# Kernel optimization log

Hardware: AMD Instinct MI355X
Metric: run time of the kernel (lower is better)

## Reference

```python
import jax, jax.numpy as jnp
import numpy as np

B, H, S, D = 4, 16, 2048, 128

def setup_inputs() -> dict:
    key = jax.random.key(0)
    k1, k2, k3, k4 = jax.random.split(key, 4)
    query = jax.random.normal(k1, (B, H, S, D), dtype=jnp.float32)
    key_t = jax.random.normal(k2, (B, H, S, D), dtype=jnp.float32)
    value = jax.random.normal(k3, (B, H, S, D), dtype=jnp.float32)
    mask = jax.random.randint(k4, (B, 1, S, S), 0, 2, dtype=jnp.int32)
    return {"query": query, "key": key_t, "value": value, "mask": mask}

def reference(query, key, value, mask):
    d_k = query.shape[-1]
    scale = d_k ** 0.5
    # [B,H,S,S] attention logits
    attn_logits = jnp.einsum('bhqd,bhkd->bhqk', query, key)
    neg_inf = jnp.finfo(attn_logits.dtype).min
    attn_logits = jnp.where(mask == 0, neg_inf, attn_logits)
    attn_weights = jax.nn.softmax(attn_logits / scale, axis=-1)
    # dropout is identity in eval/inference mode
    attn_output = jnp.einsum('bhqk,bhkd->bhqd', attn_weights, value)
    return attn_output, attn_weights
```

## Files before the change

kernel.cpp:

```cpp
#include <hip/hip_runtime.h>
#include <hip/hip_bf16.h>

namespace {

constexpr int Hn = 16;
constexpr int Sn = 2048;
constexpr int Dn = 128;
constexpr int BM = 64;
constexpr int BN = 64;
constexpr int THREADS = 256;
constexpr int NT = Sn / BN;
constexpr long long OUT0 = 4LL * 16 * 2048 * 128;

constexpr int QSTR = 136;
constexpr int VSTR = 68;

typedef short s16x4 __attribute__((ext_vector_type(4)));
typedef float f32x4 __attribute__((ext_vector_type(4)));

__device__ __forceinline__ unsigned short f2bu(float x) {
    return __bfloat16_as_ushort(__float2bfloat16(x));
}
__device__ __forceinline__ unsigned pk2(float lo, float hi) {
    return (unsigned)f2bu(lo) | ((unsigned)f2bu(hi) << 16);
}

__device__ __forceinline__ void k_issue(const float* __restrict__ g, int sc, int sr,
                                        float4* v) {
#pragma unroll
    for (int it = 0; it < 4; ++it) {
        const float4* gp = reinterpret_cast<const float4*>(
            g + (size_t)(sr + 16 * it) * Dn + sc * 8);
        v[2 * it]     = gp[0];
        v[2 * it + 1] = gp[1];
    }
}
__device__ __forceinline__ void k_write(unsigned short* lds, int sc, int sr,
                                        const float4* v) {
#pragma unroll
    for (int it = 0; it < 4; ++it) {
        const int r = sr + 16 * it;
        uint4 u;
        u.x = pk2(v[2 * it].x,     v[2 * it].y);
        u.y = pk2(v[2 * it].z,     v[2 * it].w);
        u.z = pk2(v[2 * it + 1].x, v[2 * it + 1].y);
        u.w = pk2(v[2 * it + 1].z, v[2 * it + 1].w);
        *reinterpret_cast<uint4*>(reinterpret_cast<char*>(lds) + r * (QSTR * 2) + sc * 16) = u;
    }
}

__device__ __forceinline__ void v_issue(const float* __restrict__ g, int tc, int kp,
                                        float4* v) {
#pragma unroll
    for (int it = 0; it < 4; ++it) {
        const int kr = 2 * (kp + 8 * it);
        v[2 * it]     = *reinterpret_cast<const float4*>(g + (size_t)kr * Dn + 4 * tc);
        v[2 * it + 1] = *reinterpret_cast<const float4*>(g + (size_t)(kr + 1) * Dn + 4 * tc);
    }
}
__device__ __forceinline__ void v_write(unsigned short* vt, int tc, int kp,
                                        const float4* v) {
#pragma unroll
    for (int it = 0; it < 4; ++it) {
        const int kr = 2 * (kp + 8 * it);
        const float a4[4] = {v[2 * it].x, v[2 * it].y, v[2 * it].z, v[2 * it].w};
        const float b4[4] = {v[2 * it + 1].x, v[2 * it + 1].y, v[2 * it + 1].z, v[2 * it + 1].w};
#pragma unroll
        for (int j = 0; j < 4; ++j) {
            const int d = 4 * tc + j;
            *reinterpret_cast<unsigned*>(reinterpret_cast<char*>(vt) + d * (VSTR * 2) + kr * 2)
                = pk2(a4[j], b4[j]);
        }
    }
}

struct SAcc { f32x4 t[4]; };

__global__ __launch_bounds__(THREADS)
void attn_fused(const float* __restrict__ Q, const float* __restrict__ K,
                const float* __restrict__ V, const int* __restrict__ M,
                float* __restrict__ out) {
    __shared__ __align__(16) unsigned short smem[8704 * 2 + BM * VSTR];
    unsigned short* bufA = smem;
    unsigned short* bufB = smem + 8704;
    unsigned short* wlds = smem + 17408;

    const int tid  = threadIdx.x;
    const int lane = tid & 63;
    const int wv   = tid >> 6;
    const int lr   = lane & 15;
    const int lg   = lane >> 4;

    const int bh    = blockIdx.y;
    const int b     = bh >> 4;
    const int qbase = blockIdx.x * BM;

    const float* Qg = Q + ((size_t)bh * Sn + qbase) * Dn;
    const float* Kg = K + (size_t)bh * Sn * Dn;
    const float* Vg = V + (size_t)bh * Sn * Dn;
    const int*   Mg = M + ((size_t)b * Sn + qbase) * Sn;
    float*       Og = out + ((size_t)bh * Sn + qbase) * Dn;
    float*       Wg = out + OUT0 + ((size_t)bh * Sn + qbase) * Sn;

    const float scl2 = 1.4426950408889634f / 11.313708498984761f;
    const int qrow = 16 * wv + 4 * lg;

    const int sc = tid & 15, sr = tid >> 4;
    const int tc = tid & 31, kp = tid >> 5;

    const int* mrow[4];
#pragma unroll
    for (int r = 0; r < 4; ++r) mrow[r] = Mg + (size_t)(qrow + r) * Sn + lr;

    {
        float4 qv[8], kv[8];
        k_issue(Qg, sc, sr, qv);
        k_issue(Kg, sc, sr, kv);
        k_write(bufB, sc, sr, qv);
        k_write(bufA, sc, sr, kv);
    }
    __syncthreads();
    s16x4 qf[8];
#pragma unroll
    for (int dsv = 0; dsv < 8; ++dsv)
        qf[dsv] = *reinterpret_cast<const s16x4*>(
            reinterpret_cast<const char*>(bufB) + (16 * wv + lr) * (QSTR * 2) + dsv * 32 + lg * 8);
    __syncthreads();

    const f32x4 zero = {0.f, 0.f, 0.f, 0.f};

    auto qk_tile = [&](const unsigned short* kb) -> SAcc {
        SAcc s;
#pragma unroll
        for (int t = 0; t < 4; ++t) s.t[t] = zero;
#pragma unroll
        for (int dsv = 0; dsv < 8; ++dsv) {
            const int koff = dsv * 32 + lg * 8;
#pragma unroll
            for (int t = 0; t < 4; ++t) {
                const s16x4 bb = *reinterpret_cast<const s16x4*>(
                    reinterpret_cast<const char*>(kb) + (16 * t + lr) * (QSTR * 2) + koff);
                s.t[t] = __builtin_amdgcn_mfma_f32_16x16x16bf16_1k(qf[dsv], bb, s.t[t], 0, 0, 0);
            }
        }
        return s;
    };

    float rs[4] = {0.f, 0.f, 0.f, 0.f};
    for (int t = 0; t < NT; ++t) {
        unsigned short* cur = (t & 1) ? bufB : bufA;
        unsigned short* nxt = (t & 1) ? bufA : bufB;
        float4 kv[8];
        const bool pre = (t + 1 < NT);
        if (pre) k_issue(Kg + (size_t)(t + 1) * BN * Dn, sc, sr, kv);

        int mv[16];
        const int kc = t * BN;
#pragma unroll
        for (int tt = 0; tt < 4; ++tt)
#pragma unroll
            for (int r = 0; r < 4; ++r) mv[4 * tt + r] = mrow[r][kc + 16 * tt];

        SAcc s = qk_tile(cur);
#pragma unroll
        for (int tt = 0; tt < 4; ++tt)
#pragma unroll
            for (int r = 0; r < 4; ++r)
                rs[r] += mv[4 * tt + r] ? __builtin_amdgcn_exp2f(s.t[tt][r] * scl2) : 0.f;

        if (pre) k_write(nxt, sc, sr, kv);
        __syncthreads();
    }

    float inv[4];
#pragma unroll
    for (int r = 0; r < 4; ++r) {
        float v = rs[r];
        v += __shfl_xor(v, 1);
        v += __shfl_xor(v, 2);
        v += __shfl_xor(v, 4);
        v += __shfl_xor(v, 8);
        inv[r] = 1.0f / v;
    }

    {
        float4 kv0[8], vv0[8];
        k_issue(Kg, sc, sr, kv0);
        v_issue(Vg, tc, kp, vv0);
        k_write(bufA, sc, sr, kv0);
        v_write(bufB, tc, kp, vv0);
    }
    __syncthreads();

    f32x4 oacc[8];
#pragma unroll
    for (int f = 0; f < 8; ++f) oacc[f] = zero;

    for (int t = 0; t < NT; ++t) {
        float4 kv[8], vv[8];
        const bool pre = (t + 1 < NT);
        if (pre) {
            k_issue(Kg + (size_t)(t + 1) * BN * Dn, sc, sr, kv);
            v_issue(Vg + (size_t)(t + 1) * BN * Dn, tc, kp, vv);
        }

        int mv[16];
        const int kc = t * BN;
#pragma unroll
        for (int tt = 0; tt < 4; ++tt)
#pragma unroll
            for (int r = 0; r < 4; ++r) mv[4 * tt + r] = mrow[r][kc + 16 * tt];

        SAcc s = qk_tile(bufA);

#pragma unroll
        for (int tt = 0; tt < 4; ++tt) {
#pragma unroll
            for (int r = 0; r < 4; ++r) {
                const float e = mv[4 * tt + r] ? __builtin_amdgcn_exp2f(s.t[tt][r] * scl2) : 0.f;
                const float w = e * inv[r];
                Wg[(size_t)(qrow + r) * Sn + kc + 16 * tt + lr] = w;
                reinterpret_cast<unsigned short*>(
                    reinterpret_cast<char*>(wlds) + (qrow + r) * (VSTR * 2))[16 * tt + lr] = f2bu(w);
            }
        }

#pragma unroll
        for (int kk = 0; kk < 4; ++kk) {
            const int koff = kk * 32 + lg * 8;
            const s16x4 aw = *reinterpret_cast<const s16x4*>(
                reinterpret_cast<const char*>(wlds) + (16 * wv + lr) * (VSTR * 2) + koff);
#pragma unroll
            for (int f = 0; f < 8; ++f) {
                const s16x4 bv = *reinterpret_cast<const s16x4*>(
                    reinterpret_cast<const char*>(bufB) + (16 * f + lr) * (VSTR * 2) + koff);
                oacc[f] = __builtin_amdgcn_mfma_f32_16x16x16bf16_1k(aw, bv, oacc[f], 0, 0, 0);
            }
        }
        __syncthreads();
        if (pre) {
            k_write(bufA, sc, sr, kv);
            v_write(bufB, tc, kp, vv);
        }
        __syncthreads();
    }

#pragma unroll
    for (int f = 0; f < 8; ++f) {
#pragma unroll
        for (int r = 0; r < 4; ++r) {
            Og[(size_t)(qrow + r) * Dn + 16 * f + lr] = oacc[f][r];
        }
    }
}

}

extern "C" void kernel_launch(void* const* d_in, const int* in_sizes, int n_in,
                              void* d_out, int out_size, void* d_ws, size_t ws_size,
                              hipStream_t stream) {
    (void)in_sizes; (void)n_in; (void)d_ws; (void)ws_size; (void)out_size;
    const float* Q = (const float*)d_in[0];
    const float* K = (const float*)d_in[1];
    const float* V = (const float*)d_in[2];
    const int*   M = (const int*)d_in[3];
    float* out = (float*)d_out;
    dim3 grid(Sn / BM, 4 * Hn);
    attn_fused<<<grid, THREADS, 0, stream>>>(Q, K, V, M, out);
}
```

Before: 1.006 ms.

## Shrink KV tile, bitpack mask in registers, double-buffer V, coalesce weight stores

Halves the key tile to 32 columns and adds double buffers for both K and V so one barrier per tile is enough. The mask is read once in the first pass and kept as bits in registers, so the second pass no longer reloads it from global memory. Attention weights are staged through LDS and written to global as coalesced float4 rows rather than scattered scalar stores. Block indices are remapped so blocks sharing a batch-head run close together, and launch bounds request three blocks per CU. The weights written to global now go through a bf16 round-trip, which costs some precision, and the smaller tiles add loop and barrier overhead.

New measurement: 1.510 ms. 1.5x slower.

```diff
diff --git a/kernel.cpp b/kernel.cpp
--- a/kernel.cpp
+++ b/kernel.cpp
@@ -3,17 +3,19 @@
 
 namespace {
 
-constexpr int Hn = 16;
 constexpr int Sn = 2048;
 constexpr int Dn = 128;
 constexpr int BM = 64;
-constexpr int BN = 64;
+constexpr int BN = 32;
 constexpr int THREADS = 256;
 constexpr int NT = Sn / BN;
-constexpr long long OUT0 = 4LL * 16 * 2048 * 128;
-
-constexpr int QSTR = 136;
-constexpr int VSTR = 68;
+constexpr long long OUT0 = 4LL * 16 * Sn * Dn;
+
+constexpr int KSTR = 136;
+constexpr int VSTR = 34;
+constexpr int KT = BN * KSTR;
+constexpr int VT = Dn * VSTR;
+constexpr int WT = BM * VSTR;
 
 typedef short s16x4 __attribute__((ext_vector_type(4)));
 typedef float f32x4 __attribute__((ext_vector_type(4)));
@@ -24,45 +26,48 @@
 __device__ __forceinline__ unsigned pk2(float lo, float hi) {
     return (unsigned)f2bu(lo) | ((unsigned)f2bu(hi) << 16);
 }
-
-__device__ __forceinline__ void k_issue(const float* __restrict__ g, int sc, int sr,
-                                        float4* v) {
-#pragma unroll
-    for (int it = 0; it < 4; ++it) {
+__device__ __forceinline__ float b2f(unsigned short u) {
+    union { unsigned u; float f; } v; v.u = (unsigned)u << 16; return v.f;
+}
+
+__device__ __forceinline__ void k_issue32(const float* __restrict__ g, int sc, int sr,
+                                          float4* v) {
+#pragma unroll
+    for (int it = 0; it < 2; ++it) {
         const float4* gp = reinterpret_cast<const float4*>(
             g + (size_t)(sr + 16 * it) * Dn + sc * 8);
         v[2 * it]     = gp[0];
         v[2 * it + 1] = gp[1];
     }
 }
-__device__ __forceinline__ void k_write(unsigned short* lds, int sc, int sr,
-                                        const float4* v) {
-#pragma unroll
-    for (int it = 0; it < 4; ++it) {
+__device__ __forceinline__ void k_write32(unsigned short* lds, int sc, int sr,
+                                          const float4* v) {
+#pragma unroll
+    for (int it = 0; it < 2; ++it) {
         const int r = sr + 16 * it;
         uint4 u;
         u.x = pk2(v[2 * it].x,     v[2 * it].y);
         u.y = pk2(v[2 * it].z,     v[2 * it].w);
         u.z = pk2(v[2 * it + 1].x, v[2 * it + 1].y);
         u.w = pk2(v[2 * it + 1].z, v[2 * it + 1].w);
-        *reinterpret_cast<uint4*>(reinterpret_cast<char*>(lds) + r * (QSTR * 2) + sc * 16) = u;
-    }
-}
-
-__device__ __forceinline__ void v_issue(const float* __restrict__ g, int tc, int kp,
-                                        float4* v) {
-#pragma unroll
-    for (int it = 0; it < 4; ++it) {
-        const int kr = 2 * (kp + 8 * it);
+        *reinterpret_cast<uint4*>(reinterpret_cast<char*>(lds) + r * (KSTR * 2) + sc * 16) = u;
+    }
+}
+
+__device__ __forceinline__ void v_issue32(const float* __restrict__ g, int tc, int kp,
+                                          float4* v) {
+#pragma unroll
+    for (int it = 0; it < 2; ++it) {
+        const int kr = 2 * kp + 16 * it;
         v[2 * it]     = *reinterpret_cast<const float4*>(g + (size_t)kr * Dn + 4 * tc);
         v[2 * it + 1] = *reinterpret_cast<const float4*>(g + (size_t)(kr + 1) * Dn + 4 * tc);
     }
 }
-__device__ __forceinline__ void v_write(unsigned short* vt, int tc, int kp,
-                                        const float4* v) {
-#pragma unroll
-    for (int it = 0; it < 4; ++it) {
-        const int kr = 2 * (kp + 8 * it);
+__device__ __forceinline__ void v_write32(unsigned short* vt, int tc, int kp,
+                                          const float4* v) {
+#pragma unroll
+    for (int it = 0; it < 2; ++it) {
+        const int kr = 2 * kp + 16 * it;
         const float a4[4] = {v[2 * it].x, v[2 * it].y, v[2 * it].z, v[2 * it].w};
         const float b4[4] = {v[2 * it + 1].x, v[2 * it + 1].y, v[2 * it + 1].z, v[2 * it + 1].w};
 #pragma unroll
@@ -74,16 +79,16 @@
     }
 }
 
-struct SAcc { f32x4 t[4]; };
-
-__global__ __launch_bounds__(THREADS)
+__global__ __launch_bounds__(THREADS, 3)
 void attn_fused(const float* __restrict__ Q, const float* __restrict__ K,
                 const float* __restrict__ V, const int* __restrict__ M,
                 float* __restrict__ out) {
-    __shared__ __align__(16) unsigned short smem[8704 * 2 + BM * VSTR];
-    unsigned short* bufA = smem;
-    unsigned short* bufB = smem + 8704;
-    unsigned short* wlds = smem + 17408;
+    __shared__ __align__(16) unsigned short smem[2 * KT + 2 * VT + WT];
+    unsigned short* kb0 = smem;
+    unsigned short* kb1 = smem + KT;
+    unsigned short* vb0 = smem + 2 * KT;
+    unsigned short* vb1 = smem + 2 * KT + VT;
+    unsigned short* wl  = smem + 2 * KT + 2 * VT;
 
     const int tid  = threadIdx.x;
     const int lane = tid & 63;
@@ -91,9 +96,13 @@
     const int lr   = lane & 15;
     const int lg   = lane >> 4;
 
-    const int bh    = blockIdx.y;
-    const int b     = bh >> 4;
-    const int qbase = blockIdx.x * BM;
+    const int wg = blockIdx.x;
+    const int x  = wg & 7;
+    const int j  = wg >> 3;
+    const int bh = 8 * x + (j & 7);
+    const int qt = j >> 3;
+    const int b  = bh >> 4;
+    const int qbase = qt * BM;
 
     const float* Qg = Q + ((size_t)bh * Sn + qbase) * Dn;
     const float* Kg = K + (size_t)bh * Sn * Dn;
@@ -113,63 +122,79 @@
     for (int r = 0; r < 4; ++r) mrow[r] = Mg + (size_t)(qrow + r) * Sn + lr;
 
     {
-        float4 qv[8], kv[8];
-        k_issue(Qg, sc, sr, qv);
-        k_issue(Kg, sc, sr, kv);
-        k_write(bufB, sc, sr, qv);
-        k_write(bufA, sc, sr, kv);
+        float4 q0[4], q1[4], kv[4];
+        k_issue32(Qg, sc, sr, q0);
+        k_issue32(Qg + 32 * Dn, sc, sr, q1);
+        k_issue32(Kg, sc, sr, kv);
+        k_write32(vb0, sc, sr, q0);
+        k_write32(vb1, sc, sr, q1);
+        k_write32(kb0, sc, sr, kv);
     }
     __syncthreads();
+
     s16x4 qf[8];
-#pragma unroll
-    for (int dsv = 0; dsv < 8; ++dsv)
-        qf[dsv] = *reinterpret_cast<const s16x4*>(
-            reinterpret_cast<const char*>(bufB) + (16 * wv + lr) * (QSTR * 2) + dsv * 32 + lg * 8);
+    {
+        const unsigned short* qsrc = (wv >= 2) ? vb1 : vb0;
+        const int qr = 16 * (wv & 1) + lr;
+#pragma unroll
+        for (int dsv = 0; dsv < 8; ++dsv)
+            qf[dsv] = *reinterpret_cast<const s16x4*>(
+                reinterpret_cast<const char*>(qsrc) + qr * (KSTR * 2) + dsv * 32 + lg * 8);
+    }
     __syncthreads();
 
     const f32x4 zero = {0.f, 0.f, 0.f, 0.f};
 
-    auto qk_tile = [&](const unsigned short* kb) -> SAcc {
-        SAcc s;
-#pragma unroll
-        for (int t = 0; t < 4; ++t) s.t[t] = zero;
-#pragma unroll
-        for (int dsv = 0; dsv < 8; ++dsv) {
-            const int koff = dsv * 32 + lg * 8;
-#pragma unroll
-            for (int t = 0; t < 4; ++t) {
-                const s16x4 bb = *reinterpret_cast<const s16x4*>(
-                    reinterpret_cast<const char*>(kb) + (16 * t + lr) * (QSTR * 2) + koff);
-                s.t[t] = __builtin_amdgcn_mfma_f32_16x16x16bf16_1k(qf[dsv], bb, s.t[t], 0, 0, 0);
+    float rs[4] = {0.f, 0.f, 0.f, 0.f};
+    unsigned mb[4][4];
+#pragma unroll
+    for (int r = 0; r < 4; ++r)
+#pragma unroll
+        for (int w = 0; w < 4; ++w) mb[r][w] = 0u;
+
+    {
+        unsigned short* kcur = kb0;
+        unsigned short* knxt = kb1;
+#pragma unroll
+        for (int w = 0; w < 4; ++w) {
+            for (int ti = 0; ti < 16; ++ti) {
+                const int to = 16 * w + ti;
+                const bool pre = (to < NT - 1);
+                float4 kv[4];
+                if (pre) k_issue32(Kg + (size_t)(to + 1) * BN * Dn, sc, sr, kv);
+
+                unsigned mvv[2][4];
+#pragma unroll
+                for (int t = 0; t < 2; ++t)
+#pragma unroll
+                    for (int r = 0; r < 4; ++r) {
+                        const unsigned m = (mrow[r][32 * to + 16 * t] != 0) ? 1u : 0u;
+                        mvv[t][r] = m;
+                        mb[r][w] |= m << (2 * ti + t);
+                    }
+
+                f32x4 s[2] = {zero, zero};
+#pragma unroll
+                for (int dsv = 0; dsv < 8; ++dsv) {
+                    const int koff = dsv * 32 + lg * 8;
+#pragma unroll
+                    for (int t = 0; t < 2; ++t) {
+                        const s16x4 bb = *reinterpret_cast<const s16x4*>(
+                            reinterpret_cast<const char*>(kcur) + (16 * t + lr) * (KSTR * 2) + koff);
+                        s[t] = __builtin_amdgcn_mfma_f32_16x16x16bf16_1k(qf[dsv], bb, s[t], 0, 0, 0);
+                    }
+                }
+#pragma unroll
+                for (int t = 0; t < 2; ++t)
+#pragma unroll
+                    for (int r = 0; r < 4; ++r)
+                        rs[r] += mvv[t][r] ? __builtin_amdgcn_exp2f(s[t][r] * scl2) : 0.f;
+
+                if (pre) k_write32(knxt, sc, sr, kv);
+                __syncthreads();
+                unsigned short* tmp = kcur; kcur = knxt; knxt = tmp;
             }
         }
-        return s;
-    };
-
-    float rs[4] = {0.f, 0.f, 0.f, 0.f};
-    for (int t = 0; t < NT; ++t) {
-        unsigned short* cur = (t & 1) ? bufB : bufA;
-        unsigned short* nxt = (t & 1) ? bufA : bufB;
-        float4 kv[8];
-        const bool pre = (t + 1 < NT);
-        if (pre) k_issue(Kg + (size_t)(t + 1) * BN * Dn, sc, sr, kv);
-
-        int mv[16];
-        const int kc = t * BN;
-#pragma unroll
-        for (int tt = 0; tt < 4; ++tt)
-#pragma unroll
-            for (int r = 0; r < 4; ++r) mv[4 * tt + r] = mrow[r][kc + 16 * tt];
-
-        SAcc s = qk_tile(cur);
-#pragma unroll
-        for (int tt = 0; tt < 4; ++tt)
-#pragma unroll
-            for (int r = 0; r < 4; ++r)
-                rs[r] += mv[4 * tt + r] ? __builtin_amdgcn_exp2f(s.t[tt][r] * scl2) : 0.f;
-
-        if (pre) k_write(nxt, sc, sr, kv);
-        __syncthreads();
     }
 
     float inv[4];
@@ -184,11 +209,11 @@
     }
 
     {
-        float4 kv0[8], vv0[8];
-        k_issue(Kg, sc, sr, kv0);
-        v_issue(Vg, tc, kp, vv0);
-        k_write(bufA, sc, sr, kv0);
-        v_write(bufB, tc, kp, vv0);
+        float4 kv[4], vv[4];
+        k_issue32(Kg, sc, sr, kv);
+        v_issue32(Vg, tc, kp, vv);
+        k_write32(kb0, sc, sr, kv);
+        v_write32(vb0, tc, kp, vv);
     }
     __syncthreads();
 
@@ -196,62 +221,88 @@
 #pragma unroll
     for (int f = 0; f < 8; ++f) oacc[f] = zero;
 
-    for (int t = 0; t < NT; ++t) {
-        float4 kv[8], vv[8];
-        const bool pre = (t + 1 < NT);
-        if (pre) {
-            k_issue(Kg + (size_t)(t + 1) * BN * Dn, sc, sr, kv);
-            v_issue(Vg + (size_t)(t + 1) * BN * Dn, tc, kp, vv);
-        }
-
-        int mv[16];
-        const int kc = t * BN;
-#pragma unroll
-        for (int tt = 0; tt < 4; ++tt)
-#pragma unroll
-            for (int r = 0; r < 4; ++r) mv[4 * tt + r] = mrow[r][kc + 16 * tt];
-
-        SAcc s = qk_tile(bufA);
-
-#pragma unroll
-        for (int tt = 0; tt < 4; ++tt) {
-#pragma unroll
-            for (int r = 0; r < 4; ++r) {
-                const float e = mv[4 * tt + r] ? __builtin_amdgcn_exp2f(s.t[tt][r] * scl2) : 0.f;
-                const float w = e * inv[r];
-                Wg[(size_t)(qrow + r) * Sn + kc + 16 * tt + lr] = w;
-                reinterpret_cast<unsigned short*>(
-                    reinterpret_cast<char*>(wlds) + (qrow + r) * (VSTR * 2))[16 * tt + lr] = f2bu(w);
+    {
+        unsigned short* kcur = kb0;
+        unsigned short* knxt = kb1;
+        unsigned short* vcur = vb0;
+        unsigned short* vnxt = vb1;
+        const int rowl = lane >> 2;
+        const int colg = lane & 3;
+#pragma unroll
+        for (int w = 0; w < 4; ++w) {
+            for (int ti = 0; ti < 16; ++ti) {
+                const int to = 16 * w + ti;
+                const int kc = 32 * to;
+                const bool pre = (to < NT - 1);
+                float4 kv[4], vv[4];
+                if (pre) {
+                    k_issue32(Kg + (size_t)(to + 1) * BN * Dn, sc, sr, kv);
+                    v_issue32(Vg + (size_t)(to + 1) * BN * Dn, tc, kp, vv);
+                }
+
+                f32x4 s[2] = {zero, zero};
+#pragma unroll
+                for (int dsv = 0; dsv < 8; ++dsv) {
+                    const int koff = dsv * 32 + lg * 8;
+#pragma unroll
+                    for (int t = 0; t < 2; ++t) {
+                        const s16x4 bb = *reinterpret_cast<const s16x4*>(
+                            reinterpret_cast<const char*>(kcur) + (16 * t + lr) * (KSTR * 2) + koff);
+                        s[t] = __builtin_amdgcn_mfma_f32_16x16x16bf16_1k(qf[dsv], bb, s[t], 0, 0, 0);
+                    }
+                }
+
+#pragma unroll
+                for (int t = 0; t < 2; ++t)
+#pragma unroll
+                    for (int r = 0; r < 4; ++r) {
+                        const unsigned mv = (mb[r][w] >> (2 * ti + t)) & 1u;
+                        const float e = mv ? __builtin_amdgcn_exp2f(s[t][r] * scl2) : 0.f;
+                        reinterpret_cast<unsigned short*>(
+                            reinterpret_cast<char*>(wl) + (qrow + r) * (VSTR * 2))[16 * t + lr]
+                            = f2bu(e * inv[r]);
+                    }
+
+#pragma unroll
+                for (int kk = 0; kk < 2; ++kk) {
+                    const int koff = kk * 32 + lg * 8;
+                    const s16x4 aw = *reinterpret_cast<const s16x4*>(
+                        reinterpret_cast<const char*>(wl) + (16 * wv + lr) * (VSTR * 2) + koff);
+#pragma unroll
+                    for (int f = 0; f < 8; ++f) {
+                        const s16x4 bv = *reinterpret_cast<const s16x4*>(
+                            reinterpret_cast<const char*>(vcur) + (16 * f + lr) * (VSTR * 2) + koff);
+                        oacc[f] = __builtin_amdgcn_mfma_f32_16x16x16bf16_1k(aw, bv, oacc[f], 0, 0, 0);
+                    }
+                }
+
+#pragma unroll
+                for (int i = 0; i < 2; ++i) {
+                    const ushort4 u = *reinterpret_cast<const ushort4*>(
+                        reinterpret_cast<const char*>(wl)
+                        + (16 * wv + rowl) * (VSTR * 2) + colg * 8 + 32 * i);
+                    float4 o;
+                    o.x = b2f(u.x); o.y = b2f(u.y); o.z = b2f(u.z); o.w = b2f(u.w);
+                    *reinterpret_cast<float4*>(
+                        Wg + (size_t)(16 * wv + rowl) * Sn + kc + colg * 4 + 16 * i) = o;
+                }
+
+                if (pre) {
+                    k_write32(knxt, sc, sr, kv);
+                    v_write32(vnxt, tc, kp, vv);
+                }
+                __syncthreads();
+                unsigned short* tmp = kcur; kcur = knxt; knxt = tmp;
+                tmp = vcur; vcur = vnxt; vnxt = tmp;
             }
         }
-
-#pragma unroll
-        for (int kk = 0; kk < 4; ++kk) {
-            const int koff = kk * 32 + lg * 8;
-            const s16x4 aw = *reinterpret_cast<const s16x4*>(
-                reinterpret_cast<const char*>(wlds) + (16 * wv + lr) * (VSTR * 2) + koff);
-#pragma unroll
-            for (int f = 0; f < 8; ++f) {
-                const s16x4 bv = *reinterpret_cast<const s16x4*>(
-                    reinterpret_cast<const char*>(bufB) + (16 * f + lr) * (VSTR * 2) + koff);
-                oacc[f] = __builtin_amdgcn_mfma_f32_16x16x16bf16_1k(aw, bv, oacc[f], 0, 0, 0);
-            }
-        }
-        __syncthreads();
-        if (pre) {
-            k_write(bufA, sc, sr, kv);
-            v_write(bufB, tc, kp, vv);
-        }
-        __syncthreads();
-    }
-
-#pragma unroll
-    for (int f = 0; f < 8; ++f) {
-#pragma unroll
-        for (int r = 0; r < 4; ++r) {
+    }
+
+#pragma unroll
+    for (int f = 0; f < 8; ++f)
+#pragma unroll
+        for (int r = 0; r < 4; ++r)
             Og[(size_t)(qrow + r) * Dn + 16 * f + lr] = oacc[f][r];
-        }
-    }
 }
 
 }
@@ -265,6 +316,5 @@
     const float* V = (const float*)d_in[2];
     const int*   M = (const int*)d_in[3];
     float* out = (float*)d_out;
-    dim3 grid(Sn / BM, 4 * Hn);
-    attn_fused<<<grid, THREADS, 0, stream>>>(Q, K, V, M, out);
-}
+    attn_fused<<<dim3(2048), dim3(THREADS), 0, stream>>>(Q, K, V, M, out);
+}
```

## Double query tile to 128 rows with 512 threads, fold scale into Q

Applied to the files above, without the earlier changes.

Each block now handles 128 query rows with 8 waves, so every K and V tile loaded into LDS serves twice as many rows and global K/V traffic per output halves. The softmax scale is pre-multiplied into Q during the bf16 conversion, and normalisation uses exp2(s - log2(sum)) instead of a multiply by the reciprocal. The LDS layout changes to one K buffer plus a transposed V buffer with a new stride, and launch bounds request 4 blocks per CU. Risks are higher register pressure and LDS use per block, fewer blocks in the grid, and slightly different bf16 rounding of the scaled Q.

Result: slower. 1.404 ms (+39.6%).

```diff
diff --git a/kernel.cpp b/kernel.cpp
--- a/kernel.cpp
+++ b/kernel.cpp
@@ -3,17 +3,19 @@
 
 namespace {
 
-constexpr int Hn = 16;
 constexpr int Sn = 2048;
 constexpr int Dn = 128;
-constexpr int BM = 64;
+constexpr int BM = 128;
 constexpr int BN = 64;
-constexpr int THREADS = 256;
+constexpr int THREADS = 512;
 constexpr int NT = Sn / BN;
-constexpr long long OUT0 = 4LL * 16 * 2048 * 128;
-
-constexpr int QSTR = 136;
-constexpr int VSTR = 68;
+constexpr long long OUT0 = 4LL * 16 * Sn * Dn;
+
+constexpr int KSTR = 136;
+constexpr int VSTR = 70;
+constexpr int KT = BN * KSTR;
+constexpr int VT = Dn * VSTR;
+constexpr int WT = BM * VSTR;
 
 typedef short s16x4 __attribute__((ext_vector_type(4)));
 typedef float f32x4 __attribute__((ext_vector_type(4)));
@@ -25,44 +27,57 @@
     return (unsigned)f2bu(lo) | ((unsigned)f2bu(hi) << 16);
 }
 
-__device__ __forceinline__ void k_issue(const float* __restrict__ g, int sc, int sr,
-                                        float4* v) {
-#pragma unroll
-    for (int it = 0; it < 4; ++it) {
+__device__ __forceinline__ void k_issue64(const float* __restrict__ g, int sc, int sr,
+                                          float4* v) {
+#pragma unroll
+    for (int it = 0; it < 2; ++it) {
         const float4* gp = reinterpret_cast<const float4*>(
-            g + (size_t)(sr + 16 * it) * Dn + sc * 8);
+            g + (size_t)(sr + 32 * it) * Dn + sc * 8);
         v[2 * it]     = gp[0];
         v[2 * it + 1] = gp[1];
     }
 }
-__device__ __forceinline__ void k_write(unsigned short* lds, int sc, int sr,
-                                        const float4* v) {
-#pragma unroll
-    for (int it = 0; it < 4; ++it) {
-        const int r = sr + 16 * it;
+__device__ __forceinline__ void k_write64(unsigned short* lds, int sc, int sr,
+                                          const float4* v) {
+#pragma unroll
+    for (int it = 0; it < 2; ++it) {
+        const int r = sr + 32 * it;
         uint4 u;
         u.x = pk2(v[2 * it].x,     v[2 * it].y);
         u.y = pk2(v[2 * it].z,     v[2 * it].w);
         u.z = pk2(v[2 * it + 1].x, v[2 * it + 1].y);
         u.w = pk2(v[2 * it + 1].z, v[2 * it + 1].w);
-        *reinterpret_cast<uint4*>(reinterpret_cast<char*>(lds) + r * (QSTR * 2) + sc * 16) = u;
-    }
-}
-
-__device__ __forceinline__ void v_issue(const float* __restrict__ g, int tc, int kp,
-                                        float4* v) {
-#pragma unroll
-    for (int it = 0; it < 4; ++it) {
-        const int kr = 2 * (kp + 8 * it);
+        *reinterpret_cast<uint4*>(reinterpret_cast<char*>(lds) + r * (KSTR * 2) + sc * 16) = u;
+    }
+}
+__device__ __forceinline__ void q_write64(unsigned short* lds, int sc, int sr,
+                                          const float4* v, float qs) {
+#pragma unroll
+    for (int it = 0; it < 2; ++it) {
+        const int r = sr + 32 * it;
+        uint4 u;
+        u.x = pk2(v[2 * it].x * qs,     v[2 * it].y * qs);
+        u.y = pk2(v[2 * it].z * qs,     v[2 * it].w * qs);
+        u.z = pk2(v[2 * it + 1].x * qs, v[2 * it + 1].y * qs);
+        u.w = pk2(v[2 * it + 1].z * qs, v[2 * it + 1].w * qs);
+        *reinterpret_cast<uint4*>(reinterpret_cast<char*>(lds) + r * (KSTR * 2) + sc * 16) = u;
+    }
+}
+
+__device__ __forceinline__ void v_issue64(const float* __restrict__ g, int tc, int kp,
+                                          float4* v) {
+#pragma unroll
+    for (int it = 0; it < 2; ++it) {
+        const int kr = 2 * kp + 32 * it;
         v[2 * it]     = *reinterpret_cast<const float4*>(g + (size_t)kr * Dn + 4 * tc);
         v[2 * it + 1] = *reinterpret_cast<const float4*>(g + (size_t)(kr + 1) * Dn + 4 * tc);
     }
 }
-__device__ __forceinline__ void v_write(unsigned short* vt, int tc, int kp,
-                                        const float4* v) {
-#pragma unroll
-    for (int it = 0; it < 4; ++it) {
-        const int kr = 2 * (kp + 8 * it);
+__device__ __forceinline__ void v_write64(unsigned short* vt, int tc, int kp,
+                                          const float4* v) {
+#pragma unroll
+    for (int it = 0; it < 2; ++it) {
+        const int kr = 2 * kp + 32 * it;
         const float a4[4] = {v[2 * it].x, v[2 * it].y, v[2 * it].z, v[2 * it].w};
         const float b4[4] = {v[2 * it + 1].x, v[2 * it + 1].y, v[2 * it + 1].z, v[2 * it + 1].w};
 #pragma unroll
@@ -74,16 +89,16 @@
     }
 }
 
-struct SAcc { f32x4 t[4]; };
-
-__global__ __launch_bounds__(THREADS)
+#define MFMA16(A, B, C) __builtin_amdgcn_mfma_f32_16x16x16bf16_1k((A), (B), (C), 0, 0, 0)
+
+__global__ __launch_bounds__(THREADS, 4)
 void attn_fused(const float* __restrict__ Q, const float* __restrict__ K,
                 const float* __restrict__ V, const int* __restrict__ M,
                 float* __restrict__ out) {
-    __shared__ __align__(16) unsigned short smem[8704 * 2 + BM * VSTR];
-    unsigned short* bufA = smem;
-    unsigned short* bufB = smem + 8704;
-    unsigned short* wlds = smem + 17408;
+    __shared__ __align__(16) unsigned short smem[KT + VT + WT];
+    unsigned short* kbuf = smem;
+    unsigned short* vt   = smem + KT;
+    unsigned short* wl   = smem + KT + VT;
 
     const int tid  = threadIdx.x;
     const int lane = tid & 63;
@@ -102,7 +117,7 @@
     float*       Og = out + ((size_t)bh * Sn + qbase) * Dn;
     float*       Wg = out + OUT0 + ((size_t)bh * Sn + qbase) * Sn;
 
-    const float scl2 = 1.4426950408889634f / 11.313708498984761f;
+    const float QS = 1.4426950408889634f / 11.313708498984761f;
     const int qrow = 16 * wv + 4 * lg;
 
     const int sc = tid & 15, sr = tid >> 4;
@@ -112,67 +127,72 @@
 #pragma unroll
     for (int r = 0; r < 4; ++r) mrow[r] = Mg + (size_t)(qrow + r) * Sn + lr;
 
-    {
-        float4 qv[8], kv[8];
-        k_issue(Qg, sc, sr, qv);
-        k_issue(Kg, sc, sr, kv);
-        k_write(bufB, sc, sr, qv);
-        k_write(bufA, sc, sr, kv);
-    }
-    __syncthreads();
+    const f32x4 zero = {0.f, 0.f, 0.f, 0.f};
+
+    float4 kv0[4];
+    {
+        float4 qlo[4], qhi[4];
+        k_issue64(Qg, sc, sr, qlo);
+        k_issue64(Qg + 64 * Dn, sc, sr, qhi);
+        k_issue64(Kg, sc, sr, kv0);
+        q_write64(kbuf, sc, sr, qlo, QS);
+        q_write64(vt,   sc, sr, qhi, QS);
+    }
+    __syncthreads();
+
     s16x4 qf[8];
-#pragma unroll
-    for (int dsv = 0; dsv < 8; ++dsv)
-        qf[dsv] = *reinterpret_cast<const s16x4*>(
-            reinterpret_cast<const char*>(bufB) + (16 * wv + lr) * (QSTR * 2) + dsv * 32 + lg * 8);
-    __syncthreads();
-
-    const f32x4 zero = {0.f, 0.f, 0.f, 0.f};
-
-    auto qk_tile = [&](const unsigned short* kb) -> SAcc {
-        SAcc s;
-#pragma unroll
-        for (int t = 0; t < 4; ++t) s.t[t] = zero;
-#pragma unroll
-        for (int dsv = 0; dsv < 8; ++dsv) {
-            const int koff = dsv * 32 + lg * 8;
-#pragma unroll
-            for (int t = 0; t < 4; ++t) {
-                const s16x4 bb = *reinterpret_cast<const s16x4*>(
-                    reinterpret_cast<const char*>(kb) + (16 * t + lr) * (QSTR * 2) + koff);
-                s.t[t] = __builtin_amdgcn_mfma_f32_16x16x16bf16_1k(qf[dsv], bb, s.t[t], 0, 0, 0);
-            }
-        }
-        return s;
-    };
+    {
+        const unsigned short* qsrc = (wv >= 4) ? vt : kbuf;
+        const int qr = 16 * (wv & 3) + lr;
+#pragma unroll
+        for (int dsv = 0; dsv < 8; ++dsv)
+            qf[dsv] = *reinterpret_cast<const s16x4*>(
+                reinterpret_cast<const char*>(qsrc) + qr * (KSTR * 2) + dsv * 32 + lg * 8);
+    }
+    __syncthreads();
+    k_write64(kbuf, sc, sr, kv0);
+    __syncthreads();
 
     float rs[4] = {0.f, 0.f, 0.f, 0.f};
-    for (int t = 0; t < NT; ++t) {
-        unsigned short* cur = (t & 1) ? bufB : bufA;
-        unsigned short* nxt = (t & 1) ? bufA : bufB;
-        float4 kv[8];
-        const bool pre = (t + 1 < NT);
-        if (pre) k_issue(Kg + (size_t)(t + 1) * BN * Dn, sc, sr, kv);
-
-        int mv[16];
-        const int kc = t * BN;
-#pragma unroll
-        for (int tt = 0; tt < 4; ++tt)
-#pragma unroll
-            for (int r = 0; r < 4; ++r) mv[4 * tt + r] = mrow[r][kc + 16 * tt];
-
-        SAcc s = qk_tile(cur);
-#pragma unroll
-        for (int tt = 0; tt < 4; ++tt)
-#pragma unroll
-            for (int r = 0; r < 4; ++r)
-                rs[r] += mv[4 * tt + r] ? __builtin_amdgcn_exp2f(s.t[tt][r] * scl2) : 0.f;
-
-        if (pre) k_write(nxt, sc, sr, kv);
-        __syncthreads();
-    }
-
-    float inv[4];
+    {
+        unsigned short* kcur = kbuf;
+        unsigned short* knxt = vt;
+        for (int t = 0; t < NT; ++t) {
+            const bool pre = (t + 1 < NT);
+            float4 kv[4];
+            if (pre) k_issue64(Kg + (size_t)(t + 1) * BN * Dn, sc, sr, kv);
+
+            int mv[16];
+            const int kc = t * BN;
+#pragma unroll
+            for (int tt = 0; tt < 4; ++tt)
+#pragma unroll
+                for (int r = 0; r < 4; ++r) mv[4 * tt + r] = mrow[r][kc + 16 * tt];
+
+            f32x4 s[4] = {zero, zero, zero, zero};
+#pragma unroll
+            for (int dsv = 0; dsv < 8; ++dsv) {
+                const int koff = dsv * 32 + lg * 8;
+#pragma unroll
+                for (int tt = 0; tt < 4; ++tt) {
+                    const s16x4 bb = *reinterpret_cast<const s16x4*>(
+                        reinterpret_cast<const char*>(kcur) + (16 * tt + lr) * (KSTR * 2) + koff);
+                    s[tt] = MFMA16(qf[dsv], bb, s[tt]);
+                }
+            }
+#pragma unroll
+            for (int tt = 0; tt < 4; ++tt)
+#pragma unroll
+                for (int r = 0; r < 4; ++r)
+                    rs[r] += mv[4 * tt + r] ? __builtin_amdgcn_exp2f(s[tt][r]) : 0.f;
+
+            if (pre) k_write64(knxt, sc, sr, kv);
+            __syncthreads();
+            unsigned short* tmp = kcur; kcur = knxt; knxt = tmp;
+        }
+    }
+
+    float li[4];
 #pragma unroll
     for (int r = 0; r < 4; ++r) {
         float v = rs[r];
@@ -180,15 +200,15 @@
         v += __shfl_xor(v, 2);
         v += __shfl_xor(v, 4);
         v += __shfl_xor(v, 8);
-        inv[r] = 1.0f / v;
-    }
-
-    {
-        float4 kv0[8], vv0[8];
-        k_issue(Kg, sc, sr, kv0);
-        v_issue(Vg, tc, kp, vv0);
-        k_write(bufA, sc, sr, kv0);
-        v_write(bufB, tc, kp, vv0);
+        li[r] = -__log2f(v);
+    }
+
+    {
+        float4 kv[4], vv[4];
+        k_issue64(Kg, sc, sr, kv);
+        v_issue64(Vg, tc, kp, vv);
+        k_write64(kbuf, sc, sr, kv);
+        v_write64(vt, tc, kp, vv);
     }
     __syncthreads();
 
@@ -197,31 +217,41 @@
     for (int f = 0; f < 8; ++f) oacc[f] = zero;
 
     for (int t = 0; t < NT; ++t) {
-        float4 kv[8], vv[8];
+        const int kc = t * BN;
         const bool pre = (t + 1 < NT);
+        float4 kv[4], vv[4];
         if (pre) {
-            k_issue(Kg + (size_t)(t + 1) * BN * Dn, sc, sr, kv);
-            v_issue(Vg + (size_t)(t + 1) * BN * Dn, tc, kp, vv);
+            k_issue64(Kg + (size_t)(t + 1) * BN * Dn, sc, sr, kv);
+            v_issue64(Vg + (size_t)(t + 1) * BN * Dn, tc, kp, vv);
         }
 
         int mv[16];
-        const int kc = t * BN;
 #pragma unroll
         for (int tt = 0; tt < 4; ++tt)
 #pragma unroll
             for (int r = 0; r < 4; ++r) mv[4 * tt + r] = mrow[r][kc + 16 * tt];
 
-        SAcc s = qk_tile(bufA);
+        f32x4 s[4] = {zero, zero, zero, zero};
+#pragma unroll
+        for (int dsv = 0; dsv < 8; ++dsv) {
+            const int koff = dsv * 32 + lg * 8;
+#pragma unroll
+            for (int tt = 0; tt < 4; ++tt) {
+                const s16x4 bb = *reinterpret_cast<const s16x4*>(
+                    reinterpret_cast<const char*>(kbuf) + (16 * tt + lr) * (KSTR * 2) + koff);
+                s[tt] = MFMA16(qf[dsv], bb, s[tt]);
+            }
+        }
 
 #pragma unroll
         for (int tt = 0; tt < 4; ++tt) {
 #pragma unroll
             for (int r = 0; r < 4; ++r) {
-                const float e = mv[4 * tt + r] ? __builtin_amdgcn_exp2f(s.t[tt][r] * scl2) : 0.f;
-                const float w = e * inv[r];
-                Wg[(size_t)(qrow + r) * Sn + kc + 16 * tt + lr] = w;
+                const float e = mv[4 * tt + r]
+                    ? __builtin_amdgcn_exp2f(s[tt][r] + li[r]) : 0.f;
+                Wg[(size_t)(qrow + r) * Sn + kc + 16 * tt + lr] = e;
                 reinterpret_cast<unsigned short*>(
-                    reinterpret_cast<char*>(wlds) + (qrow + r) * (VSTR * 2))[16 * tt + lr] = f2bu(w);
+                    reinterpret_cast<char*>(wl) + (qrow + r) * (VSTR * 2))[16 * tt + lr] = f2bu(e);
             }
         }
 
@@ -229,29 +259,28 @@
         for (int kk = 0; kk < 4; ++kk) {
             const int koff = kk * 32 + lg * 8;
             const s16x4 aw = *reinterpret_cast<const s16x4*>(
-                reinterpret_cast<const char*>(wlds) + (16 * wv + lr) * (VSTR * 2) + koff);
+                reinterpret_cast<const char*>(wl) + (16 * wv + lr) * (VSTR * 2) + koff);
 #pragma unroll
             for (int f = 0; f < 8; ++f) {
                 const s16x4 bv = *reinterpret_cast<const s16x4*>(
-                    reinterpret_cast<const char*>(bufB) + (16 * f + lr) * (VSTR * 2) + koff);
-                oacc[f] = __builtin_amdgcn_mfma_f32_16x16x16bf16_1k(aw, bv, oacc[f], 0, 0, 0);
-            }
-        }
+                    reinterpret_cast<const char*>(vt) + (16 * f + lr) * (VSTR * 2) + koff);
+                oacc[f] = MFMA16(aw, bv, oacc[f]);
+            }
+        }
+
         __syncthreads();
         if (pre) {
-            k_write(bufA, sc, sr, kv);
-            v_write(bufB, tc, kp, vv);
+            k_write64(kbuf, sc, sr, kv);
+            v_write64(vt, tc, kp, vv);
         }
         __syncthreads();
     }
 
 #pragma unroll
-    for (int f = 0; f < 8; ++f) {
-#pragma unroll
-        for (int r = 0; r < 4; ++r) {
+    for (int f = 0; f < 8; ++f)
+#pragma unroll
+        for (int r = 0; r < 4; ++r)
             Og[(size_t)(qrow + r) * Dn + 16 * f + lr] = oacc[f][r];
-        }
-    }
 }
 
 }
@@ -265,6 +294,6 @@
     const float* V = (const float*)d_in[2];
     const int*   M = (const int*)d_in[3];
     float* out = (float*)d_out;
-    dim3 grid(Sn / BM, 4 * Hn);
-    attn_fused<<<grid, THREADS, 0, stream>>>(Q, K, V, M, out);
-}
+    dim3 grid(Sn / BM, 4 * 16);
+    attn_fused<<<grid, dim3(THREADS), 0, stream>>>(Q, K, V, M, out);
+}
```
